# Optimization experiments

Hardware: AMD Instinct MI355X
Metric: run time of the kernel (lower is better)

## Reference

```python
import jax, jax.numpy as jnp
import numpy as np

N = 100000   # num nodes
D = 128      # node_emb_dim
R = 8        # num_relations
E = 1600000  # num edges


def setup_inputs() -> dict:
    key = jax.random.key(0)
    k0, k1, k2, k3, k4 = jax.random.split(key, 5)
    x = jax.random.normal(k0, (N, D), dtype=jnp.float32)
    edge_index = jax.random.randint(k1, (2, E), 0, N, dtype=jnp.int32)
    edge_type = jax.random.randint(k2, (E,), 0, R, dtype=jnp.int32)
    scale = 1.0 / np.sqrt(D)
    W = (jax.random.normal(k3, (R, D, D), dtype=jnp.float32) * scale)       # per-relation weight
    W_root = (jax.random.normal(k4, (D, D), dtype=jnp.float32) * scale)     # root (self-loop) weight
    bias = jnp.zeros((D,), dtype=jnp.float32)
    return {"x": x, "W": W, "W_root": W_root, "bias": bias,
            "edge_index": edge_index, "edge_type": edge_type}


def reference(x, W, W_root, bias, edge_index, edge_type):
    # PyG RGCNConv (num_bases=None, aggr='mean', root_weight=True, bias=True):
    # out_i = x_i @ W_root + bias + sum_r mean_{j in N_r(i)} x_j @ W_r
    # Mean aggregation is linear, so aggregate neighbor features per (node, relation)
    # first, then apply the per-relation transform (avoids [E,D,D] intermediates).
    src, dst = edge_index[0], edge_index[1]
    seg = dst * R + edge_type                                   # [E] segment id per (dst, rel)
    cnt = jax.ops.segment_sum(jnp.ones((E,), x.dtype), seg, num_segments=N * R)  # [N*R]
    sums = jax.ops.segment_sum(x[src], seg, num_segments=N * R)                   # [N*R, D]
    mean = sums / jnp.maximum(cnt, 1.0)[:, None]                                  # [N*R, D]
    rel_out = jnp.einsum('nrd,rde->ne', mean.reshape(N, R, D), W)                 # [N, D]
    return rel_out + x @ W_root + bias
```

## Files before the change

### kernel.cpp

```cpp
#include <hip/hip_runtime.h>


constexpr int D = 128;
constexpr int R = 8;
constexpr int TILE = 2048;

typedef __bf16 bf16x8 __attribute__((ext_vector_type(8)));
typedef float  f32x4  __attribute__((ext_vector_type(4)));
typedef unsigned short u16x8 __attribute__((ext_vector_type(8)));
typedef unsigned short u16x4 __attribute__((ext_vector_type(4)));

__device__ __forceinline__ unsigned short f2bf(float f) {
    unsigned u = __builtin_bit_cast(unsigned, f);
    u += 0x7FFFu + ((u >> 16) & 1u);
    return (unsigned short)(u >> 16);
}

__global__ __launch_bounds__(256)
void xbf_kernel(const float* __restrict__ x, unsigned short* __restrict__ xbf, int nquad) {
    int stride = gridDim.x * 256;
    for (int i = blockIdx.x * 256 + threadIdx.x; i < nquad; i += stride) {
        float4 v = ((const float4*)x)[i];
        u16x4 o;
        o[0] = f2bf(v.x); o[1] = f2bf(v.y); o[2] = f2bf(v.z); o[3] = f2bf(v.w);
        ((u16x4*)xbf)[i] = o;
    }
}

__global__ __launch_bounds__(256)
void bcount_kernel(const int* __restrict__ dst, const int* __restrict__ et,
                   int* __restrict__ meta, int E) {
    __shared__ int cnt8[8];
    if (threadIdx.x < 8) cnt8[threadIdx.x] = 0;
    __syncthreads();
    int stride = gridDim.x * 256;
    for (int e = blockIdx.x * 256 + threadIdx.x; e < E; e += stride) {
        int seg = dst[e] * R + et[e];
        atomicAdd(&cnt8[(seg >> 7) & 7], 1);
    }
    __syncthreads();
    if (threadIdx.x < 8) atomicAdd(&meta[threadIdx.x], cnt8[threadIdx.x]);
}

__global__ void bscan_kernel(int* __restrict__ meta) {
    if (threadIdx.x == 0) {
        int cum = 0;
        for (int p = 0; p < 8; ++p) {
            meta[8 + p]  = cum;
            meta[16 + p] = cum;
            cum += meta[p];
        }
    }
}

__global__ __launch_bounds__(256)
void bucketA_kernel(const int* __restrict__ src, const int* __restrict__ dst,
                    const int* __restrict__ et, int* __restrict__ ebuf_seg,
                    int* __restrict__ ebuf_src, int* __restrict__ meta, int E) {
    __shared__ int cntw[4][8];
    __shared__ int basew[4][8];
    const int tid = threadIdx.x;
    const int w   = tid >> 6;
    for (int t0 = blockIdx.x * TILE; t0 < E; t0 += gridDim.x * TILE) {
        if (tid < 32) cntw[tid >> 3][tid & 7] = 0;
        __syncthreads();
        int seg[8], sr[8], pt[8];
        bool ok[8];
        #pragma unroll
        for (int j = 0; j < 8; ++j) {
            int e = t0 + j * 256 + tid;
            ok[j] = e < E;
            if (ok[j]) {
                seg[j] = dst[e] * R + et[e];
                sr[j]  = src[e];
                pt[j]  = (seg[j] >> 7) & 7;
                atomicAdd(&cntw[w][pt[j]], 1);
            }
        }
        __syncthreads();
        if (tid < 8) {
            int p = tid;
            int tot = cntw[0][p] + cntw[1][p] + cntw[2][p] + cntw[3][p];
            int b = atomicAdd(&meta[16 + p], tot);
            basew[0][p] = b;               b += cntw[0][p];
            basew[1][p] = b;               b += cntw[1][p];
            basew[2][p] = b;               b += cntw[2][p];
            basew[3][p] = b;
            cntw[0][p] = 0; cntw[1][p] = 0; cntw[2][p] = 0; cntw[3][p] = 0;
        }
        __syncthreads();
        #pragma unroll
        for (int j = 0; j < 8; ++j) {
            if (ok[j]) {
                int r   = atomicAdd(&cntw[w][pt[j]], 1);
                int pos = basew[w][pt[j]] + r;
                ebuf_seg[pos] = seg[j];
                ebuf_src[pos] = sr[j];
            }
        }
        __syncthreads();
    }
}

__global__ __launch_bounds__(256)
void hist_kernel(const int* __restrict__ ebuf_seg, const int* __restrict__ meta,
                 int* __restrict__ hist) {
    int part = blockIdx.x & 7;
    int nb   = gridDim.x >> 3;
    int lo   = meta[8 + part];
    int n    = meta[part];
    for (int i = (blockIdx.x >> 3) * 256 + threadIdx.x; i < n; i += nb * 256)
        atomicAdd(&hist[ebuf_seg[lo + i]], 1);
}

__global__ __launch_bounds__(256)
void block_sums_kernel(const int* __restrict__ hs, int* __restrict__ bsum, int n) {
    __shared__ int sh[256];
    int i = blockIdx.x * 256 + threadIdx.x;
    sh[threadIdx.x] = (i < n) ? hs[i] : 0;
    __syncthreads();
    for (int off = 128; off > 0; off >>= 1) {
        if (threadIdx.x < off) sh[threadIdx.x] += sh[threadIdx.x + off];
        __syncthreads();
    }
    if (threadIdx.x == 0) bsum[blockIdx.x] = sh[0];
}

__global__ __launch_bounds__(64)
void scan_bsum_kernel(int* __restrict__ bsum, int nb) {
    int lane = threadIdx.x;
    int carry = 0;
    for (int base = 0; base < nb; base += 64) {
        int i = base + lane;
        int orig = (i < nb) ? bsum[i] : 0;
        int v = orig;
        #pragma unroll
        for (int off = 1; off < 64; off <<= 1) {
            int u = __shfl_up(v, off, 64);
            if (lane >= off) v += u;
        }
        int tot = __shfl(v, 63, 64);
        if (i < nb) bsum[i] = carry + (v - orig);
        carry += tot;
    }
}

__global__ __launch_bounds__(256)
void scan_block_kernel(int* __restrict__ hs, const int* __restrict__ bsum,
                       int* __restrict__ cursor, int n, int E) {
    __shared__ int sh[256];
    int tid = threadIdx.x;
    int i = blockIdx.x * 256 + tid;
    int v = (i < n) ? hs[i] : 0;
    sh[tid] = v;
    __syncthreads();
    for (int off = 1; off < 256; off <<= 1) {
        int u = (tid >= off) ? sh[tid - off] : 0;
        __syncthreads();
        sh[tid] += u;
        __syncthreads();
    }
    int st = bsum[blockIdx.x] + sh[tid] - v;
    if (i < n) { hs[i] = st; cursor[i] = st; }
    if (i == n) hs[n] = E;
}

__global__ __launch_bounds__(256)
void bucketB_kernel(const int* __restrict__ ebuf_seg, const int* __restrict__ ebuf_src,
                    const int* __restrict__ meta, int* __restrict__ cursor,
                    int* __restrict__ spack) {
    int part = blockIdx.x & 7;
    int nb   = gridDim.x >> 3;
    int lo   = meta[8 + part];
    int n    = meta[part];
    for (int i = (blockIdx.x >> 3) * 256 + threadIdx.x; i < n; i += nb * 256) {
        int seg = ebuf_seg[lo + i];
        int s   = ebuf_src[lo + i];
        int pos = atomicAdd(&cursor[seg], 1);
        spack[pos] = s;
    }
}

__global__ __launch_bounds__(256)
void aggregate_kernel(const unsigned short* __restrict__ xbf,
                      const int* __restrict__ spack,
                      const int* __restrict__ hstart,
                      unsigned short* __restrict__ mean,
                      int nseg, int tshift, int c0) {
    int idx = blockIdx.x * 256 + threadIdx.x;
    int seg = idx >> tshift;
    int c8  = idx & ((1 << tshift) - 1);
    if (seg >= nseg) return;
    int p0 = hstart[seg], p1 = hstart[seg + 1];
    int coff = c0 + c8 * 8;
    float a[8] = {};
    for (int p = p0; p < p1; ++p) {
        int s = spack[p];
        u16x8 v = *(const u16x8*)(xbf + ((size_t)s << 7) + coff);
        #pragma unroll
        for (int j = 0; j < 8; ++j)
            a[j] += __builtin_bit_cast(float, (unsigned)v[j] << 16);
    }
    float inv = (p1 > p0) ? 1.0f / (float)(p1 - p0) : 0.0f;
    u16x8 o;
    #pragma unroll
    for (int j = 0; j < 8; ++j) o[j] = f2bf(a[j] * inv);
    __builtin_nontemporal_store(o, (u16x8*)(mean + ((size_t)seg << (tshift + 3)) + c8 * 8));
}

__global__ __launch_bounds__(256)
void wallt_kernel(const float* __restrict__ Wroot, const float* __restrict__ W,
                  unsigned short* __restrict__ WallTc, int KW, int CW, int c0, int first) {
    int idx = blockIdx.x * 256 + threadIdx.x;
    if (idx >= 128 * KW) return;
    int n = idx / KW, kk = idx % KW;
    float v;
    if (first && kk < 128) {
        v = Wroot[kk * 128 + n];
    } else {
        int lk = kk - (first ? 128 : 0);
        int r = lk / CW, cc = lk % CW;
        v = W[((size_t)r * 128 + c0 + cc) * 128 + n];
    }
    WallTc[idx] = f2bf(v);
}

template<bool FIRST>
__global__ __launch_bounds__(256)
void mfma_gemm_kernel(const unsigned short* __restrict__ xbf,
                      const unsigned short* __restrict__ mean,
                      const unsigned short* __restrict__ WallTc,
                      const float* __restrict__ bias,
                      float* __restrict__ out,
                      int N, int NT, int KW, int MROW) {
    __shared__ unsigned short As[128][32];
    __shared__ unsigned short Bs[128][32];
    const int tid  = threadIdx.x;
    const int row0 = blockIdx.x * 128;
    const int lane = tid & 63;
    const int wid  = tid >> 6;
    const int wm   = wid >> 1;
    const int wn   = wid & 1;
    const int srow = tid >> 1;
    const int sh16 = (tid & 1) * 16;

    f32x4 acc[4][4] = {};

    const int  node = row0 + srow;
    const bool nok  = node < N;

    for (int kt = 0; kt < NT; ++kt) {
        if (kt) __syncthreads();
        u16x8 a0, a1;
        #pragma unroll
        for (int j = 0; j < 8; ++j) { a0[j] = 0; a1[j] = 0; }
        if (FIRST && kt < 4) {
            if (nok) {
                const u16x8* xp = (const u16x8*)(xbf + ((size_t)node << 7) + kt * 32 + sh16);
                a0 = xp[0]; a1 = xp[1];
            }
        } else {
            if (nok) {
                const u16x8* mp = (const u16x8*)(mean + (size_t)node * MROW
                                                 + (kt - (FIRST ? 4 : 0)) * 32 + sh16);
                a0 = mp[0]; a1 = mp[1];
            }
        }
        const u16x8* wp = (const u16x8*)(WallTc + (size_t)srow * KW + kt * 32 + sh16);
        u16x8 b0 = wp[0], b1 = wp[1];

        *(u16x8*)&As[srow][sh16]     = a0;
        *(u16x8*)&As[srow][sh16 + 8] = a1;
        *(u16x8*)&Bs[srow][sh16]     = b0;
        *(u16x8*)&Bs[srow][sh16 + 8] = b1;
        __syncthreads();

        const int kg = (lane >> 4) * 8;
        const int rl = lane & 15;
        bf16x8 av[4], bv[4];
        #pragma unroll
        for (int f = 0; f < 4; ++f) {
            av[f] = __builtin_bit_cast(bf16x8, *(const u16x8*)&As[wm * 64 + f * 16 + rl][kg]);
            bv[f] = __builtin_bit_cast(bf16x8, *(const u16x8*)&Bs[wn * 64 + f * 16 + rl][kg]);
        }
        #pragma unroll
        for (int mf = 0; mf < 4; ++mf)
            #pragma unroll
            for (int nf = 0; nf < 4; ++nf)
                acc[mf][nf] = __builtin_amdgcn_mfma_f32_16x16x32_bf16(av[mf], bv[nf],
                                                                     acc[mf][nf], 0, 0, 0);
    }

    const int rl = lane & 15;
    const int rg = lane >> 4;
    #pragma unroll
    for (int nf = 0; nf < 4; ++nf) {
        int n = wn * 64 + nf * 16 + rl;
        float bb = FIRST ? bias[n] : 0.0f;
        #pragma unroll
        for (int mf = 0; mf < 4; ++mf) {
            #pragma unroll
            for (int i = 0; i < 4; ++i) {
                int nd = row0 + wm * 64 + mf * 16 + rg * 4 + i;
                if (nd < N) {
                    size_t o = (size_t)nd * 128 + n;
                    if (FIRST) out[o] = acc[mf][nf][i] + bb;
                    else       out[o] += acc[mf][nf][i];
                }
            }
        }
    }
}

extern "C" void kernel_launch(void* const* d_in, const int* in_sizes, int n_in,
                              void* d_out, int out_size, void* d_ws, size_t ws_size,
                              hipStream_t stream) {
    const float* x     = (const float*)d_in[0];
    const float* W     = (const float*)d_in[1];
    const float* Wroot = (const float*)d_in[2];
    const float* bias  = (const float*)d_in[3];
    const int*   ei    = (const int*)d_in[4];
    const int*   et    = (const int*)d_in[5];
    float*       out   = (float*)d_out;

    const int N = in_sizes[0] / D;
    const int E = in_sizes[5];
    const int* src = ei;
    const int* dst = ei + E;

    const int NSEG = N * R;
    const int NB   = (NSEG + 256) / 256;

    const size_t xbf_bytes    = (size_t)N * D * 2;
    const size_t walltc_bytes = (size_t)128 * 1152 * 2;
    const size_t fixed_bytes  = xbf_bytes + walltc_bytes +
                                ((size_t)(NSEG + 1) + NSEG + E + NB + 32) * 4 + 256;

    int CW = 0, tshift = 0;
    const int cands[3]   = {128, 64, 32};
    const int tshifts[3] = {4, 3, 2};
    for (int i = 0; i < 3; ++i) {
        size_t need = (size_t)NSEG * cands[i] * 2 + fixed_bytes;
        if (need <= ws_size) { CW = cands[i]; tshift = tshifts[i]; break; }
    }
    if (CW == 0) return;

    char* p = (char*)d_ws;
    unsigned short* mean   = (unsigned short*)p;  p += (size_t)NSEG * CW * 2;
    unsigned short* xbf    = (unsigned short*)p;  p += xbf_bytes;
    unsigned short* WallTc = (unsigned short*)p;  p += walltc_bytes;
    int* hstart = (int*)p;  p += (size_t)(NSEG + 1) * 4;
    int* cursor = (int*)p;  p += (size_t)NSEG * 4;
    int* spack  = (int*)p;  p += (size_t)E * 4;
    int* bsum   = (int*)p;  p += (size_t)NB * 4;
    int* meta   = (int*)p;

    int* ebuf_seg = (int*)mean;
    int* ebuf_src = ebuf_seg + E;

    hipMemsetAsync(hstart, 0, (size_t)(NSEG + 1) * 4, stream);
    hipMemsetAsync(meta, 0, 32 * 4, stream);

    xbf_kernel<<<2048, 256, 0, stream>>>(x, xbf, N * D / 4);

    bcount_kernel<<<1024, 256, 0, stream>>>(dst, et, meta, E);
    bscan_kernel<<<1, 64, 0, stream>>>(meta);
    bucketA_kernel<<<(E + TILE - 1) / TILE, 256, 0, stream>>>(
        src, dst, et, ebuf_seg, ebuf_src, meta, E);
    hist_kernel<<<768, 256, 0, stream>>>(ebuf_seg, meta, hstart);
    block_sums_kernel<<<NB, 256, 0, stream>>>(hstart, bsum, NSEG);
    scan_bsum_kernel<<<1, 64, 0, stream>>>(bsum, NB);
    scan_block_kernel<<<NB, 256, 0, stream>>>(hstart, bsum, cursor, NSEG, E);
    bucketB_kernel<<<768, 256, 0, stream>>>(ebuf_seg, ebuf_src, meta, cursor, spack);

    const int gx  = (N + 127) / 128;
    const int nch = D / CW;
    for (int c = 0; c < nch; ++c) {
        int c0    = c * CW;
        int first = (c == 0);
        long long aggth = (long long)NSEG << tshift;
        aggregate_kernel<<<(int)((aggth + 255) / 256), 256, 0, stream>>>(
            xbf, spack, hstart, mean, NSEG, tshift, c0);
        int KW   = (first ? 128 : 0) + R * CW;
        int NT   = KW / 32;
        int MROW = R * CW;
        wallt_kernel<<<(128 * KW + 255) / 256, 256, 0, stream>>>(
            Wroot, W, WallTc, KW, CW, c0, first);
        if (first)
            mfma_gemm_kernel<true><<<gx, 256, 0, stream>>>(
                xbf, mean, WallTc, bias, out, N, NT, KW, MROW);
        else
            mfma_gemm_kernel<false><<<gx, 256, 0, stream>>>(
                xbf, mean, WallTc, bias, out, N, NT, KW, MROW);
    }
}
```

Measured before the change: 435.7 us.

## Fix channel chunking, fuse histogram into count, shrink GEMM tile, unroll gather

Channel-chunk width is fixed at 64, so the pipeline always runs two aggregate+GEMM passes, and the edge buffers get their own workspace instead of aliasing the mean buffer. The per-segment histogram moves into the bucket-count kernel, which removes a separate pass over the bucketed edges at the cost of scattered global atomics on unsorted segments. The gather loop is unrolled by four to keep more loads in flight, and the mean store is now a normal store instead of nontemporal. The GEMM tile shrinks to 64 rows with padded LDS rows to cut bank conflicts and raise occupancy, at the cost of reloading the weight tile for twice as many blocks.

```diff
diff --git a/kernel.cpp b/kernel.cpp
--- a/kernel.cpp
+++ b/kernel.cpp
@@ -4,6 +4,8 @@
 constexpr int D = 128;
 constexpr int R = 8;
 constexpr int TILE = 2048;
+constexpr int CW = 64;
+constexpr int LDA = 40;
 
 typedef __bf16 bf16x8 __attribute__((ext_vector_type(8)));
 typedef float  f32x4  __attribute__((ext_vector_type(4)));
@@ -14,6 +16,9 @@
     unsigned u = __builtin_bit_cast(unsigned, f);
     u += 0x7FFFu + ((u >> 16) & 1u);
     return (unsigned short)(u >> 16);
+}
+__device__ __forceinline__ float bf2f(unsigned short h) {
+    return __builtin_bit_cast(float, (unsigned)h << 16);
 }
 
 __global__ __launch_bounds__(256)
@@ -29,7 +34,7 @@
 
 __global__ __launch_bounds__(256)
 void bcount_kernel(const int* __restrict__ dst, const int* __restrict__ et,
-                   int* __restrict__ meta, int E) {
+                   int* __restrict__ meta, int* __restrict__ hist, int E) {
     __shared__ int cnt8[8];
     if (threadIdx.x < 8) cnt8[threadIdx.x] = 0;
     __syncthreads();
@@ -37,6 +42,7 @@
     for (int e = blockIdx.x * 256 + threadIdx.x; e < E; e += stride) {
         int seg = dst[e] * R + et[e];
         atomicAdd(&cnt8[(seg >> 7) & 7], 1);
+        atomicAdd(&hist[seg], 1);
     }
     __syncthreads();
     if (threadIdx.x < 8) atomicAdd(&meta[threadIdx.x], cnt8[threadIdx.x]);
@@ -100,17 +106,6 @@
         }
         __syncthreads();
     }
-}
-
-__global__ __launch_bounds__(256)
-void hist_kernel(const int* __restrict__ ebuf_seg, const int* __restrict__ meta,
-                 int* __restrict__ hist) {
-    int part = blockIdx.x & 7;
-    int nb   = gridDim.x >> 3;
-    int lo   = meta[8 + part];
-    int n    = meta[part];
-    for (int i = (blockIdx.x >> 3) * 256 + threadIdx.x; i < n; i += nb * 256)
-        atomicAdd(&hist[ebuf_seg[lo + i]], 1);
 }
 
 __global__ __launch_bounds__(256)
@@ -186,31 +181,48 @@
                       const int* __restrict__ spack,
                       const int* __restrict__ hstart,
                       unsigned short* __restrict__ mean,
-                      int nseg, int tshift, int c0) {
+                      int nseg, int c0) {
     int idx = blockIdx.x * 256 + threadIdx.x;
-    int seg = idx >> tshift;
-    int c8  = idx & ((1 << tshift) - 1);
+    int seg = idx >> 3;
+    int c8  = idx & 7;
     if (seg >= nseg) return;
     int p0 = hstart[seg], p1 = hstart[seg + 1];
     int coff = c0 + c8 * 8;
     float a[8] = {};
-    for (int p = p0; p < p1; ++p) {
-        int s = spack[p];
-        u16x8 v = *(const u16x8*)(xbf + ((size_t)s << 7) + coff);
-        #pragma unroll
-        for (int j = 0; j < 8; ++j)
-            a[j] += __builtin_bit_cast(float, (unsigned)v[j] << 16);
+    for (int p = p0; p < p1; p += 4) {
+        int s0 = spack[p];
+        int s1 = (p + 1 < p1) ? spack[p + 1] : -1;
+        int s2 = (p + 2 < p1) ? spack[p + 2] : -1;
+        int s3 = (p + 3 < p1) ? spack[p + 3] : -1;
+        u16x8 v0 = *(const u16x8*)(xbf + ((size_t)s0 << 7) + coff);
+        #pragma unroll
+        for (int j = 0; j < 8; ++j) a[j] += bf2f(v0[j]);
+        if (s1 >= 0) {
+            u16x8 v = *(const u16x8*)(xbf + ((size_t)s1 << 7) + coff);
+            #pragma unroll
+            for (int j = 0; j < 8; ++j) a[j] += bf2f(v[j]);
+        }
+        if (s2 >= 0) {
+            u16x8 v = *(const u16x8*)(xbf + ((size_t)s2 << 7) + coff);
+            #pragma unroll
+            for (int j = 0; j < 8; ++j) a[j] += bf2f(v[j]);
+        }
+        if (s3 >= 0) {
+            u16x8 v = *(const u16x8*)(xbf + ((size_t)s3 << 7) + coff);
+            #pragma unroll
+            for (int j = 0; j < 8; ++j) a[j] += bf2f(v[j]);
+        }
     }
     float inv = (p1 > p0) ? 1.0f / (float)(p1 - p0) : 0.0f;
     u16x8 o;
     #pragma unroll
     for (int j = 0; j < 8; ++j) o[j] = f2bf(a[j] * inv);
-    __builtin_nontemporal_store(o, (u16x8*)(mean + ((size_t)seg << (tshift + 3)) + c8 * 8));
+    *(u16x8*)(mean + ((size_t)seg << 6) + c8 * 8) = o;
 }
 
 __global__ __launch_bounds__(256)
 void wallt_kernel(const float* __restrict__ Wroot, const float* __restrict__ W,
-                  unsigned short* __restrict__ WallTc, int KW, int CW, int c0, int first) {
+                  unsigned short* __restrict__ WallTc, int KW, int c0, int first) {
     int idx = blockIdx.x * 256 + threadIdx.x;
     if (idx >= 128 * KW) return;
     int n = idx / KW, kk = idx % KW;
@@ -233,61 +245,60 @@
                       const float* __restrict__ bias,
                       float* __restrict__ out,
                       int N, int NT, int KW, int MROW) {
-    __shared__ unsigned short As[128][32];
-    __shared__ unsigned short Bs[128][32];
+    __shared__ unsigned short As[64 * LDA];
+    __shared__ unsigned short Bs[128 * LDA];
     const int tid  = threadIdx.x;
-    const int row0 = blockIdx.x * 128;
+    const int nd0  = blockIdx.x * 64;
     const int lane = tid & 63;
     const int wid  = tid >> 6;
     const int wm   = wid >> 1;
     const int wn   = wid & 1;
-    const int srow = tid >> 1;
-    const int sh16 = (tid & 1) * 16;
-
-    f32x4 acc[4][4] = {};
-
-    const int  node = row0 + srow;
-    const bool nok  = node < N;
+    const int arow = tid >> 2;
+    const int aoct = tid & 3;
+    const int brow = tid >> 1;
+    const int bhalf = tid & 1;
+
+    f32x4 acc[2][4] = {};
+
+    const int  anode = nd0 + arow;
+    const bool aok   = anode < N;
 
     for (int kt = 0; kt < NT; ++kt) {
         if (kt) __syncthreads();
-        u16x8 a0, a1;
-        #pragma unroll
-        for (int j = 0; j < 8; ++j) { a0[j] = 0; a1[j] = 0; }
-        if (FIRST && kt < 4) {
-            if (nok) {
-                const u16x8* xp = (const u16x8*)(xbf + ((size_t)node << 7) + kt * 32 + sh16);
-                a0 = xp[0]; a1 = xp[1];
-            }
-        } else {
-            if (nok) {
-                const u16x8* mp = (const u16x8*)(mean + (size_t)node * MROW
-                                                 + (kt - (FIRST ? 4 : 0)) * 32 + sh16);
-                a0 = mp[0]; a1 = mp[1];
-            }
-        }
-        const u16x8* wp = (const u16x8*)(WallTc + (size_t)srow * KW + kt * 32 + sh16);
+        u16x8 av8;
+        #pragma unroll
+        for (int j = 0; j < 8; ++j) av8[j] = 0;
+        if (aok) {
+            if (FIRST && kt < 4)
+                av8 = *(const u16x8*)(xbf + ((size_t)anode << 7) + kt * 32 + aoct * 8);
+            else
+                av8 = *(const u16x8*)(mean + (size_t)anode * MROW
+                                      + (kt - (FIRST ? 4 : 0)) * 32 + aoct * 8);
+        }
+        const u16x8* wp = (const u16x8*)(WallTc + (size_t)brow * KW + kt * 32 + bhalf * 16);
         u16x8 b0 = wp[0], b1 = wp[1];
 
-        *(u16x8*)&As[srow][sh16]     = a0;
-        *(u16x8*)&As[srow][sh16 + 8] = a1;
-        *(u16x8*)&Bs[srow][sh16]     = b0;
-        *(u16x8*)&Bs[srow][sh16 + 8] = b1;
-        __syncthreads();
-
-        const int kg = (lane >> 4) * 8;
+        *(u16x8*)&As[arow * LDA + aoct * 8]            = av8;
+        *(u16x8*)&Bs[brow * LDA + bhalf * 16]          = b0;
+        *(u16x8*)&Bs[brow * LDA + bhalf * 16 + 8]      = b1;
+        __syncthreads();
+
+        const int ko = (lane >> 4) * 8;
         const int rl = lane & 15;
-        bf16x8 av[4], bv[4];
-        #pragma unroll
-        for (int f = 0; f < 4; ++f) {
-            av[f] = __builtin_bit_cast(bf16x8, *(const u16x8*)&As[wm * 64 + f * 16 + rl][kg]);
-            bv[f] = __builtin_bit_cast(bf16x8, *(const u16x8*)&Bs[wn * 64 + f * 16 + rl][kg]);
-        }
-        #pragma unroll
-        for (int mf = 0; mf < 4; ++mf)
+        bf16x8 af[2], bf[4];
+        #pragma unroll
+        for (int f = 0; f < 2; ++f)
+            af[f] = __builtin_bit_cast(bf16x8,
+                *(const u16x8*)&As[(wm * 32 + f * 16 + rl) * LDA + ko]);
+        #pragma unroll
+        for (int f = 0; f < 4; ++f)
+            bf[f] = __builtin_bit_cast(bf16x8,
+                *(const u16x8*)&Bs[(wn * 64 + f * 16 + rl) * LDA + ko]);
+        #pragma unroll
+        for (int mf = 0; mf < 2; ++mf)
             #pragma unroll
             for (int nf = 0; nf < 4; ++nf)
-                acc[mf][nf] = __builtin_amdgcn_mfma_f32_16x16x32_bf16(av[mf], bv[nf],
+                acc[mf][nf] = __builtin_amdgcn_mfma_f32_16x16x32_bf16(af[mf], bf[nf],
                                                                      acc[mf][nf], 0, 0, 0);
     }
 
@@ -298,10 +309,10 @@
         int n = wn * 64 + nf * 16 + rl;
         float bb = FIRST ? bias[n] : 0.0f;
         #pragma unroll
-        for (int mf = 0; mf < 4; ++mf) {
+        for (int mf = 0; mf < 2; ++mf) {
             #pragma unroll
             for (int i = 0; i < 4; ++i) {
-                int nd = row0 + wm * 64 + mf * 16 + rg * 4 + i;
+                int nd = nd0 + wm * 32 + mf * 16 + rg * 4 + i;
                 if (nd < N) {
                     size_t o = (size_t)nd * 128 + n;
                     if (FIRST) out[o] = acc[mf][nf][i] + bb;
@@ -331,61 +342,50 @@
     const int NSEG = N * R;
     const int NB   = (NSEG + 256) / 256;
 
+    const size_t mean_bytes   = (size_t)NSEG * CW * 2;
     const size_t xbf_bytes    = (size_t)N * D * 2;
-    const size_t walltc_bytes = (size_t)128 * 1152 * 2;
-    const size_t fixed_bytes  = xbf_bytes + walltc_bytes +
-                                ((size_t)(NSEG + 1) + NSEG + E + NB + 32) * 4 + 256;
-
-    int CW = 0, tshift = 0;
-    const int cands[3]   = {128, 64, 32};
-    const int tshifts[3] = {4, 3, 2};
-    for (int i = 0; i < 3; ++i) {
-        size_t need = (size_t)NSEG * cands[i] * 2 + fixed_bytes;
-        if (need <= ws_size) { CW = cands[i]; tshift = tshifts[i]; break; }
-    }
-    if (CW == 0) return;
+    const size_t walltc_bytes = (size_t)128 * 640 * 2;
+    const size_t need = mean_bytes + xbf_bytes + walltc_bytes +
+                        ((size_t)(NSEG + 1) + NSEG + E + NB + 32 + 2 * (size_t)E) * 4 + 256;
+    if (ws_size < need) return;
 
     char* p = (char*)d_ws;
-    unsigned short* mean   = (unsigned short*)p;  p += (size_t)NSEG * CW * 2;
+    unsigned short* mean   = (unsigned short*)p;  p += mean_bytes;
     unsigned short* xbf    = (unsigned short*)p;  p += xbf_bytes;
     unsigned short* WallTc = (unsigned short*)p;  p += walltc_bytes;
-    int* hstart = (int*)p;  p += (size_t)(NSEG + 1) * 4;
-    int* cursor = (int*)p;  p += (size_t)NSEG * 4;
-    int* spack  = (int*)p;  p += (size_t)E * 4;
-    int* bsum   = (int*)p;  p += (size_t)NB * 4;
-    int* meta   = (int*)p;
-
-    int* ebuf_seg = (int*)mean;
-    int* ebuf_src = ebuf_seg + E;
+    int* hstart   = (int*)p;  p += (size_t)(NSEG + 1) * 4;
+    int* cursor   = (int*)p;  p += (size_t)NSEG * 4;
+    int* spack    = (int*)p;  p += (size_t)E * 4;
+    int* bsum     = (int*)p;  p += (size_t)NB * 4;
+    int* meta     = (int*)p;  p += 32 * 4;
+    int* ebuf_seg = (int*)p;  p += (size_t)E * 4;
+    int* ebuf_src = (int*)p;
 
     hipMemsetAsync(hstart, 0, (size_t)(NSEG + 1) * 4, stream);
     hipMemsetAsync(meta, 0, 32 * 4, stream);
 
     xbf_kernel<<<2048, 256, 0, stream>>>(x, xbf, N * D / 4);
 
-    bcount_kernel<<<1024, 256, 0, stream>>>(dst, et, meta, E);
+    bcount_kernel<<<1024, 256, 0, stream>>>(dst, et, meta, hstart, E);
     bscan_kernel<<<1, 64, 0, stream>>>(meta);
     bucketA_kernel<<<(E + TILE - 1) / TILE, 256, 0, stream>>>(
         src, dst, et, ebuf_seg, ebuf_src, meta, E);
-    hist_kernel<<<768, 256, 0, stream>>>(ebuf_seg, meta, hstart);
     block_sums_kernel<<<NB, 256, 0, stream>>>(hstart, bsum, NSEG);
     scan_bsum_kernel<<<1, 64, 0, stream>>>(bsum, NB);
     scan_block_kernel<<<NB, 256, 0, stream>>>(hstart, bsum, cursor, NSEG, E);
     bucketB_kernel<<<768, 256, 0, stream>>>(ebuf_seg, ebuf_src, meta, cursor, spack);
 
-    const int gx  = (N + 127) / 128;
-    const int nch = D / CW;
-    for (int c = 0; c < nch; ++c) {
+    const int gx = (N + 63) / 64;
+    for (int c = 0; c < 2; ++c) {
         int c0    = c * CW;
         int first = (c == 0);
-        long long aggth = (long long)NSEG << tshift;
-        aggregate_kernel<<<(int)((aggth + 255) / 256), 256, 0, stream>>>(
-            xbf, spack, hstart, mean, NSEG, tshift, c0);
+        aggregate_kernel<<<(NSEG * 8 + 255) / 256, 256, 0, stream>>>(
+            xbf, spack, hstart, mean, NSEG, c0);
         int KW   = (first ? 128 : 0) + R * CW;
         int NT   = KW / 32;
         int MROW = R * CW;
         wallt_kernel<<<(128 * KW + 255) / 256, 256, 0, stream>>>(
-            Wroot, W, WallTc, KW, CW, c0, first);
+            Wroot, W, WallTc, KW, c0, first);
         if (first)
             mfma_gemm_kernel<true><<<gx, 256, 0, stream>>>(
                 xbf, mean, WallTc, bias, out, N, NT, KW, MROW);
```

Result: faster. 416.6 us (-4.4%).
